# Kernel tuning notes

Measured on AMD Instinct MI355X. Metric: run time of the kernel, lower is better.

Reference implementation:

```python
import jax, jax.numpy as jnp
import numpy as np

B, S, D_IN = 2, 2048, 1024
D_OUT, HEADS = 1024, 16
HD = D_OUT // HEADS  # head_dim = 64


def rope_sincos(seq_len, head_dim):
    half = head_dim // 2
    inv_freq = 1.0 / (10000.0 ** (jnp.arange(half, dtype=jnp.float32) / half))
    angles = jnp.arange(seq_len, dtype=jnp.float32)[:, None] * inv_freq[None, :]  # (s, hd/2)
    return jnp.sin(angles), jnp.cos(angles)


def apply_rope(x, sin, cos):
    # x: (b, h, s, hd); interleaved-pair rotation as in the torch module
    b, h, s, hd = x.shape
    xp = x.reshape(b, h, s, hd // 2, 2)
    x0, x1 = xp[..., 0], xp[..., 1]
    sin = sin[:s][None, None, :, :]
    cos = cos[:s][None, None, :, :]
    r0 = x0 * cos - x1 * sin
    r1 = x0 * sin + x1 * cos
    return jnp.stack([r0, r1], axis=-1).reshape(b, h, s, hd)


def setup_inputs() -> dict:
    key = jax.random.key(0)
    kx, kq, kk, kv, ko = jax.random.split(key, 5)
    scale = 0.02
    return {
        "x": jax.random.normal(kx, (B, S, D_IN), dtype=jnp.float32),
        "Wq": jax.random.normal(kq, (D_IN, D_OUT), dtype=jnp.float32) * scale,
        "Wk": jax.random.normal(kk, (D_IN, D_OUT), dtype=jnp.float32) * scale,
        "Wv": jax.random.normal(kv, (D_IN, D_OUT), dtype=jnp.float32) * scale,
        "Wo": jax.random.normal(ko, (D_OUT, D_OUT), dtype=jnp.float32) * scale,
    }


def reference(x, Wq, Wk, Wv, Wo):
    b, s, _ = x.shape
    q = (x @ Wq).reshape(b, s, HEADS, HD).transpose(0, 2, 1, 3)  # (b,h,s,hd)
    k = (x @ Wk).reshape(b, s, HEADS, HD).transpose(0, 2, 1, 3)
    v = (x @ Wv).reshape(b, s, HEADS, HD).transpose(0, 2, 1, 3)
    sin, cos = rope_sincos(s, HD)
    q = apply_rope(q, sin, cos)
    k = apply_rope(k, sin, cos)
    scores = jnp.einsum('bhqd,bhkd->bhqk', q, k)
    causal = jnp.triu(jnp.ones((s, s), dtype=bool), 1)
    scores = jnp.where(causal[None, None], -jnp.inf, scores)
    weights = jax.nn.softmax(scores / jnp.sqrt(jnp.float32(HD)), axis=-1)
    ctx = jnp.einsum('bhqk,bhkd->bhqd', weights, v)
    ctx = ctx.transpose(0, 2, 1, 3).reshape(b, s, D_OUT)
    return ctx @ Wo
```

## Files before the change

### kernel.cpp

```cpp
#include <hip/hip_runtime.h>
#include <cstdint>
#include <cstddef>

#define BB 2
#define SS 2048
#define DD 1024
#define HH 16
#define HDD 64

typedef unsigned short u16;
typedef unsigned int u32;
typedef __attribute__((ext_vector_type(8))) short bf16x8;
typedef __attribute__((ext_vector_type(4))) float f32x4;

__device__ __forceinline__ u16 f2bf(float f) {
    union { float f; u32 u; } c; c.f = f;
    u32 r = c.u + 0x7fffu + ((c.u >> 16) & 1u);
    return (u16)(r >> 16);
}
__device__ __forceinline__ void gll16(const void* g, void* l) {
    __builtin_amdgcn_global_load_lds(
        (const __attribute__((address_space(1))) void*)g,
        (__attribute__((address_space(3))) void*)l, 16, 0, 0);
}

__global__ __launch_bounds__(256) void cvt_x(const float* __restrict__ X, u16* __restrict__ Xb)
{
    const int idx0 = blockIdx.x * 256 + threadIdx.x;
    #pragma unroll
    for (int i = 0; i < 4; i++) {
        const int c = idx0 + i * 262144;
        const float4 v = *(const float4*)&X[(size_t)c * 4];
        ushort4 o;
        o.x = f2bf(v.x); o.y = f2bf(v.y); o.z = f2bf(v.z); o.w = f2bf(v.w);
        *(ushort4*)&Xb[(size_t)c * 4] = o;
    }
}

__global__ __launch_bounds__(256) void trans_w4(
    const float* Wq, const float* Wk, const float* Wv, const float* Wo,
    u16* __restrict__ WTbase)
{
    __shared__ float L[32][33];
    const float* Ws[4] = {Wq, Wk, Wv, Wo};
    const float* W = Ws[blockIdx.z];
    u16* WT = WTbase + (size_t)blockIdx.z * (DD * DD);
    const int k0 = blockIdx.x * 32, n0 = blockIdx.y * 32;
    const int tx = threadIdx.x & 31, ty = threadIdx.x >> 5;
    #pragma unroll
    for (int i = 0; i < 4; i++)
        L[ty + 8 * i][tx] = W[(size_t)(k0 + ty + 8 * i) * DD + n0 + tx];
    __syncthreads();
    #pragma unroll
    for (int i = 0; i < 4; i++) {
        const int n = ty + 8 * i;
        WT[(size_t)(n0 + n) * DD + k0 + tx] = f2bf(L[tx][n]);
    }
}

__global__ __launch_bounds__(256) void gemm_qkv(
    const u16* __restrict__ Xb, const u16* __restrict__ WTall, u16* __restrict__ QKVb)
{
    __shared__ __align__(16) u16 sm[16384];
    const int tid = threadIdx.x;
    const int lane = tid & 63;
    const int w = tid >> 6;
    const int li = lane & 15, quad = lane >> 4;
    const int wr = w >> 1, wc = w & 1;
    const int which = blockIdx.x >> 3;
    const int n0 = (blockIdx.x & 7) * 128;
    const int m0 = blockIdx.y * 64;
    const u16* BT = WTall + (size_t)which * (DD * DD);
    u16* outp = QKVb + (size_t)which * ((size_t)BB * HH * SS * HDD);
    const float scale = (which == 0) ? 0.125f * 1.4426950408889634f : 1.0f;

    const int arow = tid >> 2;
    const int acol = (tid & 3) * 8;
    const int wbase = (tid >> 6) * 1024;

    auto stage = [&](int t, int buf) {
        char* base = (char*)(sm + buf * 6144);
        const int k0 = t * 32;
        gll16(Xb + (size_t)(m0 + arow) * DD + k0 + acol, base + wbase);
        #pragma unroll
        for (int rr = 0; rr < 2; rr++)
            gll16(BT + (size_t)(n0 + rr * 64 + arow) * DD + k0 + acol,
                  base + 4096 + rr * 4096 + wbase);
    };

    f32x4 acc[2][4] = {};
    stage(0, 0);
    __syncthreads();
    for (int t = 0; t < 32; t++) {
        const int buf = t & 1;
        if (t < 31) stage(t + 1, buf ^ 1);
        const u16* tA = sm + buf * 6144;
        const u16* tB = tA + 2048;
        bf16x8 a[2], b[4];
        #pragma unroll
        for (int f = 0; f < 2; f++)
            a[f] = *(const bf16x8*)(tA + (wr * 32 + f * 16 + li) * 32 + quad * 8);
        #pragma unroll
        for (int f = 0; f < 4; f++)
            b[f] = *(const bf16x8*)(tB + (wc * 64 + f * 16 + li) * 32 + quad * 8);
        #pragma unroll
        for (int fm = 0; fm < 2; fm++)
            #pragma unroll
            for (int fn = 0; fn < 4; fn++)
                acc[fm][fn] = __builtin_amdgcn_mfma_f32_16x16x32_bf16(
                    a[fm], b[fn], acc[fm][fn], 0, 0, 0);
        __syncthreads();
    }

    const int bidx = m0 >> 11;
    const int s0 = m0 & (SS - 1);
    if (which < 2) {
        float (*Ts)[128] = (float(*)[128])sm;
        #pragma unroll
        for (int fm = 0; fm < 2; fm++)
            #pragma unroll
            for (int fn = 0; fn < 4; fn++)
                #pragma unroll
                for (int r = 0; r < 4; r++)
                    Ts[wr * 32 + fm * 16 + quad * 4 + r][wc * 64 + fn * 16 + li] = acc[fm][fn][r];
        __syncthreads();
        #pragma unroll
        for (int i = 0; i < 4; i++) {
            const int c = tid + 256 * i;
            const int mr = c >> 4;
            const int nc = c & 15;
            const int s = s0 + mr;
            const int n = n0 + nc * 8;
            const int h = n >> 6, hd0 = n & 63;
            const float4 v0 = *(const float4*)&Ts[mr][nc * 8];
            const float4 v1 = *(const float4*)&Ts[mr][nc * 8 + 4];
            const float fs = (float)s;
            u32 w0, w1, w2, w3;
            {
                const float inv = exp2f((float)((hd0 >> 1) + 0) * -0.4152410118609203f);
                float sn, cs; sincosf(fs * inv, &sn, &cs);
                w0 = (u32)f2bf((v0.x * cs - v0.y * sn) * scale) |
                     ((u32)f2bf((v0.x * sn + v0.y * cs) * scale) << 16);
            }
            {
                const float inv = exp2f((float)((hd0 >> 1) + 1) * -0.4152410118609203f);
                float sn, cs; sincosf(fs * inv, &sn, &cs);
                w1 = (u32)f2bf((v0.z * cs - v0.w * sn) * scale) |
                     ((u32)f2bf((v0.z * sn + v0.w * cs) * scale) << 16);
            }
            {
                const float inv = exp2f((float)((hd0 >> 1) + 2) * -0.4152410118609203f);
                float sn, cs; sincosf(fs * inv, &sn, &cs);
                w2 = (u32)f2bf((v1.x * cs - v1.y * sn) * scale) |
                     ((u32)f2bf((v1.x * sn + v1.y * cs) * scale) << 16);
            }
            {
                const float inv = exp2f((float)((hd0 >> 1) + 3) * -0.4152410118609203f);
                float sn, cs; sincosf(fs * inv, &sn, &cs);
                w3 = (u32)f2bf((v1.z * cs - v1.w * sn) * scale) |
                     ((u32)f2bf((v1.z * sn + v1.w * cs) * scale) << 16);
            }
            uint4 ov; ov.x = w0; ov.y = w1; ov.z = w2; ov.w = w3;
            *(uint4*)&outp[((size_t)(bidx * HH + h) * SS + s) * HDD + hd0] = ov;
        }
    } else {
        float (*Ts)[64] = (float(*)[64])sm;
        #pragma unroll
        for (int fm = 0; fm < 2; fm++)
            #pragma unroll
            for (int fn = 0; fn < 4; fn++)
                *(float4*)&Ts[wc * 64 + fn * 16 + li][wr * 32 + fm * 16 + quad * 4] =
                    make_float4(acc[fm][fn][0], acc[fm][fn][1],
                                acc[fm][fn][2], acc[fm][fn][3]);
        __syncthreads();
        #pragma unroll
        for (int i = 0; i < 4; i++) {
            const int c = tid + 256 * i;
            const int nr = c >> 3;
            const int mc = c & 7;
            const int n = n0 + nr;
            const int h = n >> 6, hd = n & 63;
            const float4 v0 = *(const float4*)&Ts[nr][mc * 8];
            const float4 v1 = *(const float4*)&Ts[nr][mc * 8 + 4];
            uint4 ov;
            ov.x = (u32)f2bf(v0.x) | ((u32)f2bf(v0.y) << 16);
            ov.y = (u32)f2bf(v0.z) | ((u32)f2bf(v0.w) << 16);
            ov.z = (u32)f2bf(v1.x) | ((u32)f2bf(v1.y) << 16);
            ov.w = (u32)f2bf(v1.z) | ((u32)f2bf(v1.w) << 16);
            *(uint4*)&outp[((size_t)(bidx * HH + h) * HDD + hd) * SS + s0 + mc * 8] = ov;
        }
    }
}

__global__ __launch_bounds__(512) void attn_mfma(
    const u16* __restrict__ Qb, const u16* __restrict__ Kb,
    const u16* __restrict__ Vt, u16* __restrict__ ctxb)
{
    __shared__ u16 Ks[128][72];
    __shared__ u16 Vs[64][136];
    __shared__ u16 Ps[8][16][136];
    const int tid = threadIdx.x;
    const int lane = tid & 63;
    const int w = tid >> 6;
    const int li = lane & 15;
    const int quad = lane >> 4;
    const int bh = blockIdx.y;
    const int i = blockIdx.x;
    const int q0A = 128 * i;
    const int q0B = 128 * (15 - i);
    const int ntA = i + 1;
    const int ntB = 16 - i;

    bf16x8 aQA0, aQA1, aQB0, aQB1;
    {
        const u16* qa = Qb + ((size_t)bh * SS + q0A + 16 * w + li) * HDD + quad * 8;
        aQA0 = *(const bf16x8*)qa;
        aQA1 = *(const bf16x8*)(qa + 32);
        const u16* qb = Qb + ((size_t)bh * SS + q0B + 16 * w + li) * HDD + quad * 8;
        aQB0 = *(const bf16x8*)qb;
        aQB1 = *(const bf16x8*)(qb + 32);
    }

    f32x4 OA[4] = {}, OB[4] = {};
    float lA[4] = {}, lB[4] = {};

    const int kr = tid >> 2;
    const int kc = (tid & 3) * 16;
    const int vr = tid >> 3;
    const int vc = (tid & 7) * 16;

    auto process = [&](const bf16x8& aQ0, const bf16x8& aQ1,
                       f32x4 (&O)[4], float (&l_r)[4], const bool diag) {
        f32x4 S[8];
        #pragma unroll
        for (int t = 0; t < 8; t++) {
            const bf16x8 b0 = *(const bf16x8*)&Ks[16 * t + li][quad * 8];
            const bf16x8 b1 = *(const bf16x8*)&Ks[16 * t + li][32 + quad * 8];
            f32x4 a2 = {};
            a2 = __builtin_amdgcn_mfma_f32_16x16x32_bf16(aQ0, b0, a2, 0, 0, 0);
            a2 = __builtin_amdgcn_mfma_f32_16x16x32_bf16(aQ1, b1, a2, 0, 0, 0);
            S[t] = a2;
        }
        if (diag) {
            #pragma unroll
            for (int t = 0; t < 8; t++)
                #pragma unroll
                for (int r = 0; r < 4; r++)
                    if (16 * t + li > 16 * w + quad * 4 + r) S[t][r] = -1e30f;
        }
        float p[4][8];
        #pragma unroll
        for (int r = 0; r < 4; r++) {
            float ls = 0.f;
            #pragma unroll
            for (int t = 0; t < 8; t++) {
                p[r][t] = exp2f(S[t][r] - 8.0f);
                ls += p[r][t];
            }
            l_r[r] += ls;
        }
        #pragma unroll
        for (int r = 0; r < 4; r++)
            #pragma unroll
            for (int t = 0; t < 8; t++)
                Ps[w][quad * 4 + r][16 * t + li] = f2bf(p[r][t]);
        bf16x8 aP[4];
        #pragma unroll
        for (int c = 0; c < 4; c++)
            aP[c] = *(const bf16x8*)&Ps[w][li][32 * c + quad * 8];
        #pragma unroll
        for (int t2 = 0; t2 < 4; t2++) {
            #pragma unroll
            for (int c = 0; c < 4; c++) {
                const bf16x8 bv = *(const bf16x8*)&Vs[16 * t2 + li][32 * c + quad * 8];
                O[t2] = __builtin_amdgcn_mfma_f32_16x16x32_bf16(aP[c], bv, O[t2], 0, 0, 0);
            }
        }
    };

    for (int jt = 0; jt < ntB; jt++) {
        const int j0 = jt << 7;
        const uint4 k0v = *(const uint4*)(Kb + ((size_t)bh * SS + j0 + kr) * HDD + kc);
        const uint4 k1v = *(const uint4*)(Kb + ((size_t)bh * SS + j0 + kr) * HDD + kc + 8);
        const uint4 v0v = *(const uint4*)(Vt + ((size_t)bh * HDD + vr) * SS + j0 + vc);
        const uint4 v1v = *(const uint4*)(Vt + ((size_t)bh * HDD + vr) * SS + j0 + vc + 8);
        __syncthreads();
        *(uint4*)&Ks[kr][kc] = k0v;
        *(uint4*)&Ks[kr][kc + 8] = k1v;
        *(uint4*)&Vs[vr][vc] = v0v;
        *(uint4*)&Vs[vr][vc + 8] = v1v;
        __syncthreads();

        if (jt < ntA) process(aQA0, aQA1, OA, lA, jt == ntA - 1);
        process(aQB0, aQB1, OB, lB, jt == ntB - 1);
    }

    const int b = bh >> 4, h = bh & 15;
    #pragma unroll
    for (int r = 0; r < 4; r++) {
        float la = lA[r], lb = lB[r];
        #pragma unroll
        for (int off = 1; off < 16; off <<= 1) {
            la += __shfl_xor(la, off);
            lb += __shfl_xor(lb, off);
        }
        const float invA = 1.f / la;
        const float invB = 1.f / lb;
        const int rowA = q0A + 16 * w + quad * 4 + r;
        const int rowB = q0B + 16 * w + quad * 4 + r;
        #pragma unroll
        for (int t2 = 0; t2 < 4; t2++) {
            ctxb[((size_t)b * SS + rowA) * DD + h * HDD + 16 * t2 + li] = f2bf(OA[t2][r] * invA);
            ctxb[((size_t)b * SS + rowB) * DD + h * HDD + 16 * t2 + li] = f2bf(OB[t2][r] * invB);
        }
    }
}

__global__ __launch_bounds__(256) void gemm_out_mfma(
    const u16* __restrict__ Ab, const u16* __restrict__ WoT, float* __restrict__ out)
{
    __shared__ __align__(16) u16 sm[12288];
    const int tid = threadIdx.x;
    const int lane = tid & 63;
    const int w = tid >> 6;
    const int li = lane & 15, quad = lane >> 4;
    const int wr = w >> 1, wc = w & 1;
    const int n0 = blockIdx.x * 128;
    const int m0 = blockIdx.y * 64;

    const int arow = tid >> 2;
    const int acol = (tid & 3) * 8;
    const int wbase = (tid >> 6) * 1024;

    auto stage = [&](int t, int buf) {
        char* base = (char*)(sm + buf * 6144);
        const int k0 = t * 32;
        gll16(Ab + (size_t)(m0 + arow) * DD + k0 + acol, base + wbase);
        #pragma unroll
        for (int rr = 0; rr < 2; rr++)
            gll16(WoT + (size_t)(n0 + rr * 64 + arow) * DD + k0 + acol,
                  base + 4096 + rr * 4096 + wbase);
    };

    f32x4 acc[2][4] = {};
    stage(0, 0);
    __syncthreads();
    for (int t = 0; t < 32; t++) {
        const int buf = t & 1;
        if (t < 31) stage(t + 1, buf ^ 1);
        const u16* tA = sm + buf * 6144;
        const u16* tB = tA + 2048;
        bf16x8 a[2], b[4];
        #pragma unroll
        for (int f = 0; f < 2; f++)
            a[f] = *(const bf16x8*)(tA + (wr * 32 + f * 16 + li) * 32 + quad * 8);
        #pragma unroll
        for (int f = 0; f < 4; f++)
            b[f] = *(const bf16x8*)(tB + (wc * 64 + f * 16 + li) * 32 + quad * 8);
        #pragma unroll
        for (int fm = 0; fm < 2; fm++)
            #pragma unroll
            for (int fn = 0; fn < 4; fn++)
                acc[fm][fn] = __builtin_amdgcn_mfma_f32_16x16x32_bf16(
                    a[fm], b[fn], acc[fm][fn], 0, 0, 0);
        __syncthreads();
    }

    #pragma unroll
    for (int fm = 0; fm < 2; fm++)
        #pragma unroll
        for (int r = 0; r < 4; r++) {
            const size_t mg = (size_t)(m0 + wr * 32 + fm * 16 + quad * 4 + r) * DD;
            #pragma unroll
            for (int fn = 0; fn < 4; fn++)
                out[mg + n0 + wc * 64 + fn * 16 + li] = acc[fm][fn][r];
        }
}

extern "C" void kernel_launch(void* const* d_in, const int* in_sizes, int n_in,
                              void* d_out, int out_size, void* d_ws, size_t ws_size,
                              hipStream_t stream) {
    const float* x  = (const float*)d_in[0];
    const float* Wq = (const float*)d_in[1];
    const float* Wk = (const float*)d_in[2];
    const float* Wv = (const float*)d_in[3];
    const float* Wo = (const float*)d_in[4];
    float* out = (float*)d_out;

    u16* ws16 = (u16*)d_ws;
    const size_t E = 4194304;
    const size_t M = 1048576;
    u16* QKVb = ws16;
    u16* Qb   = QKVb;
    u16* Kb   = QKVb + E;
    u16* Vt   = QKVb + 2 * E;
    u16* Xb   = ws16 + 3 * E;
    u16* ctxb = Xb;
    u16* WTall = ws16 + 4 * E;
    u16* WoT  = WTall + 3 * M;

    hipLaunchKernelGGL(cvt_x, dim3(1024), dim3(256), 0, stream, x, Xb);
    hipLaunchKernelGGL(trans_w4, dim3(32, 32, 4), dim3(256), 0, stream,
                       Wq, Wk, Wv, Wo, WTall);
    hipLaunchKernelGGL(gemm_qkv, dim3(24, 64), dim3(256), 0, stream, Xb, WTall, QKVb);
    hipLaunchKernelGGL(attn_mfma, dim3(8, BB * HH), dim3(512), 0, stream,
                       Qb, Kb, Vt, ctxb);
    hipLaunchKernelGGL(gemm_out_mfma, dim3(8, 64), dim3(256), 0, stream, ctxb, WoT, out);
}
```

Before: 205.0 us.

## Use two waves per GEMM block with larger per-wave tiles and precomputed RoPE table

```diff
diff --git a/kernel.cpp b/kernel.cpp
--- a/kernel.cpp
+++ b/kernel.cpp
@@ -58,15 +58,14 @@
     }
 }
 
-__global__ __launch_bounds__(256) void gemm_qkv(
+__global__ __launch_bounds__(128) void gemm_qkv(
     const u16* __restrict__ Xb, const u16* __restrict__ WTall, u16* __restrict__ QKVb)
 {
     __shared__ __align__(16) u16 sm[16384];
     const int tid = threadIdx.x;
     const int lane = tid & 63;
-    const int w = tid >> 6;
+    const int w2 = tid >> 6;
     const int li = lane & 15, quad = lane >> 4;
-    const int wr = w >> 1, wc = w & 1;
     const int which = blockIdx.x >> 3;
     const int n0 = (blockIdx.x & 7) * 128;
     const int m0 = blockIdx.y * 64;
@@ -74,21 +73,24 @@
     u16* outp = QKVb + (size_t)which * ((size_t)BB * HH * SS * HDD);
     const float scale = (which == 0) ? 0.125f * 1.4426950408889634f : 1.0f;
 
-    const int arow = tid >> 2;
-    const int acol = (tid & 3) * 8;
-    const int wbase = (tid >> 6) * 1024;
+    const int srow = tid >> 2;
+    const int scol = (tid & 3) * 8;
+    const int wb = w2 * 1024;
 
     auto stage = [&](int t, int buf) {
-        char* base = (char*)(sm + buf * 6144);
+        char* base = (char*)sm + buf * 12288;
         const int k0 = t * 32;
-        gll16(Xb + (size_t)(m0 + arow) * DD + k0 + acol, base + wbase);
         #pragma unroll
         for (int rr = 0; rr < 2; rr++)
-            gll16(BT + (size_t)(n0 + rr * 64 + arow) * DD + k0 + acol,
-                  base + 4096 + rr * 4096 + wbase);
+            gll16(Xb + (size_t)(m0 + rr * 32 + srow) * DD + k0 + scol,
+                  base + rr * 2048 + wb);
+        #pragma unroll
+        for (int rr = 0; rr < 4; rr++)
+            gll16(BT + (size_t)(n0 + rr * 32 + srow) * DD + k0 + scol,
+                  base + 4096 + rr * 2048 + wb);
     };
 
-    f32x4 acc[2][4] = {};
+    f32x4 acc[4][4] = {};
     stage(0, 0);
     __syncthreads();
     for (int t = 0; t < 32; t++) {
@@ -96,15 +98,14 @@
         if (t < 31) stage(t + 1, buf ^ 1);
         const u16* tA = sm + buf * 6144;
         const u16* tB = tA + 2048;
-        bf16x8 a[2], b[4];
-        #pragma unroll
-        for (int f = 0; f < 2; f++)
-            a[f] = *(const bf16x8*)(tA + (wr * 32 + f * 16 + li) * 32 + quad * 8);
-        #pragma unroll
-        for (int f = 0; f < 4; f++)
-            b[f] = *(const bf16x8*)(tB + (wc * 64 + f * 16 + li) * 32 + quad * 8);
-        #pragma unroll
-        for (int fm = 0; fm < 2; fm++)
+        bf16x8 a[4], b[4];
+        #pragma unroll
+        for (int f = 0; f < 4; f++) {
+            a[f] = *(const bf16x8*)(tA + (f * 16 + li) * 32 + quad * 8);
+            b[f] = *(const bf16x8*)(tB + (w2 * 64 + f * 16 + li) * 32 + quad * 8);
+        }
+        #pragma unroll
+        for (int fm = 0; fm < 4; fm++)
             #pragma unroll
             for (int fn = 0; fn < 4; fn++)
                 acc[fm][fn] = __builtin_amdgcn_mfma_f32_16x16x32_bf16(
@@ -115,79 +116,93 @@
     const int bidx = m0 >> 11;
     const int s0 = m0 & (SS - 1);
     if (which < 2) {
+        float* tabc = (float*)(sm + 8192);
+        float* tabs = tabc + 2048;
+        {
+            const int j = tid & 31;
+            const int sb = tid >> 5;
+            const float inv = exp2f((float)j * -0.4152410118609203f);
+            #pragma unroll
+            for (int k = 0; k < 16; k++) {
+                const int sl = k * 4 + sb;
+                float sn, cs;
+                sincosf((float)(s0 + sl) * inv, &sn, &cs);
+                tabc[sl * 32 + j] = cs;
+                tabs[sl * 32 + j] = sn;
+            }
+        }
         float (*Ts)[128] = (float(*)[128])sm;
         #pragma unroll
-        for (int fm = 0; fm < 2; fm++)
-            #pragma unroll
-            for (int fn = 0; fn < 4; fn++)
+        for (int p = 0; p < 2; p++) {
+            if (p) __syncthreads();
+            #pragma unroll
+            for (int fm2 = 0; fm2 < 2; fm2++) {
+                const int fm = p * 2 + fm2;
                 #pragma unroll
-                for (int r = 0; r < 4; r++)
-                    Ts[wr * 32 + fm * 16 + quad * 4 + r][wc * 64 + fn * 16 + li] = acc[fm][fn][r];
-        __syncthreads();
-        #pragma unroll
-        for (int i = 0; i < 4; i++) {
-            const int c = tid + 256 * i;
-            const int mr = c >> 4;
-            const int nc = c & 15;
-            const int s = s0 + mr;
-            const int n = n0 + nc * 8;
-            const int h = n >> 6, hd0 = n & 63;
-            const float4 v0 = *(const float4*)&Ts[mr][nc * 8];
-            const float4 v1 = *(const float4*)&Ts[mr][nc * 8 + 4];
-            const float fs = (float)s;
-            u32 w0, w1, w2, w3;
-            {
-                const float inv = exp2f((float)((hd0 >> 1) + 0) * -0.4152410118609203f);
-                float sn, cs; sincosf(fs * inv, &sn, &cs);
-                w0 = (u32)f2bf((v0.x * cs - v0.y * sn) * scale) |
-                     ((u32)f2bf((v0.x * sn + v0.y * cs) * scale) << 16);
-            }
-            {
-                const float inv = exp2f((float)((hd0 >> 1) + 1) * -0.4152410118609203f);
-                float sn, cs; sincosf(fs * inv, &sn, &cs);
-                w1 = (u32)f2bf((v0.z * cs - v0.w * sn) * scale) |
-                     ((u32)f2bf((v0.z * sn + v0.w * cs) * scale) << 16);
-            }
-            {
-                const float inv = exp2f((float)((hd0 >> 1) + 2) * -0.4152410118609203f);
-                float sn, cs; sincosf(fs * inv, &sn, &cs);
-                w2 = (u32)f2bf((v1.x * cs - v1.y * sn) * scale) |
-                     ((u32)f2bf((v1.x * sn + v1.y * cs) * scale) << 16);
-            }
-            {
-                const float inv = exp2f((float)((hd0 >> 1) + 3) * -0.4152410118609203f);
-                float sn, cs; sincosf(fs * inv, &sn, &cs);
-                w3 = (u32)f2bf((v1.z * cs - v1.w * sn) * scale) |
-                     ((u32)f2bf((v1.z * sn + v1.w * cs) * scale) << 16);
-            }
-            uint4 ov; ov.x = w0; ov.y = w1; ov.z = w2; ov.w = w3;
-            *(uint4*)&outp[((size_t)(bidx * HH + h) * SS + s) * HDD + hd0] = ov;
+                for (int fn = 0; fn < 4; fn++)
+                    #pragma unroll
+                    for (int r = 0; r < 4; r++)
+                        Ts[fm2 * 16 + quad * 4 + r][w2 * 64 + fn * 16 + li] = acc[fm][fn][r];
+            }
+            __syncthreads();
+            #pragma unroll
+            for (int i = 0; i < 4; i++) {
+                const int c = tid + 128 * i;
+                const int mr = c >> 4;
+                const int nc = c & 15;
+                const int sl = p * 32 + mr;
+                const int s = s0 + sl;
+                const int n = n0 + nc * 8;
+                const int h = n >> 6, hd0 = n & 63;
+                const int j0 = hd0 >> 1;
+                const float4 v0 = *(const float4*)&Ts[mr][nc * 8];
+                const float4 v1 = *(const float4*)&Ts[mr][nc * 8 + 4];
+                const float4 cs4 = *(const float4*)&tabc[sl * 32 + j0];
+                const float4 sn4 = *(const float4*)&tabs[sl * 32 + j0];
+                u32 w0, w1, w2o, w3;
+                w0 = (u32)f2bf((v0.x * cs4.x - v0.y * sn4.x) * scale) |
+                     ((u32)f2bf((v0.x * sn4.x + v0.y * cs4.x) * scale) << 16);
+                w1 = (u32)f2bf((v0.z * cs4.y - v0.w * sn4.y) * scale) |
+                     ((u32)f2bf((v0.z * sn4.y + v0.w * cs4.y) * scale) << 16);
+                w2o = (u32)f2bf((v1.x * cs4.z - v1.y * sn4.z) * scale) |
+                      ((u32)f2bf((v1.x * sn4.z + v1.y * cs4.z) * scale) << 16);
+                w3 = (u32)f2bf((v1.z * cs4.w - v1.w * sn4.w) * scale) |
+                     ((u32)f2bf((v1.z * sn4.w + v1.w * cs4.w) * scale) << 16);
+                uint4 ov; ov.x = w0; ov.y = w1; ov.z = w2o; ov.w = w3;
+                *(uint4*)&outp[((size_t)(bidx * HH + h) * SS + s) * HDD + hd0] = ov;
+            }
         }
     } else {
         float (*Ts)[64] = (float(*)[64])sm;
         #pragma unroll
-        for (int fm = 0; fm < 2; fm++)
-            #pragma unroll
-            for (int fn = 0; fn < 4; fn++)
-                *(float4*)&Ts[wc * 64 + fn * 16 + li][wr * 32 + fm * 16 + quad * 4] =
-                    make_float4(acc[fm][fn][0], acc[fm][fn][1],
-                                acc[fm][fn][2], acc[fm][fn][3]);
-        __syncthreads();
-        #pragma unroll
-        for (int i = 0; i < 4; i++) {
-            const int c = tid + 256 * i;
-            const int nr = c >> 3;
-            const int mc = c & 7;
-            const int n = n0 + nr;
-            const int h = n >> 6, hd = n & 63;
-            const float4 v0 = *(const float4*)&Ts[nr][mc * 8];
-            const float4 v1 = *(const float4*)&Ts[nr][mc * 8 + 4];
-            uint4 ov;
-            ov.x = (u32)f2bf(v0.x) | ((u32)f2bf(v0.y) << 16);
-            ov.y = (u32)f2bf(v0.z) | ((u32)f2bf(v0.w) << 16);
-            ov.z = (u32)f2bf(v1.x) | ((u32)f2bf(v1.y) << 16);
-            ov.w = (u32)f2bf(v1.z) | ((u32)f2bf(v1.w) << 16);
-            *(uint4*)&outp[((size_t)(bidx * HH + h) * HDD + hd) * SS + s0 + mc * 8] = ov;
+        for (int p = 0; p < 2; p++) {
+            if (p) __syncthreads();
+            if (w2 == p) {
+                #pragma unroll
+                for (int fm = 0; fm < 4; fm++)
+                    #pragma unroll
+                    for (int fn = 0; fn < 4; fn++)
+                        *(float4*)&Ts[fn * 16 + li][fm * 16 + quad * 4] =
+                            make_float4(acc[fm][fn][0], acc[fm][fn][1],
+                                        acc[fm][fn][2], acc[fm][fn][3]);
+            }
+            __syncthreads();
+            #pragma unroll
+            for (int i = 0; i < 4; i++) {
+                const int c = tid + 128 * i;
+                const int nr = c >> 3;
+                const int mc = c & 7;
+                const int n = n0 + p * 64 + nr;
+                const int h = n >> 6, hd = n & 63;
+                const float4 v0 = *(const float4*)&Ts[nr][mc * 8];
+                const float4 v1 = *(const float4*)&Ts[nr][mc * 8 + 4];
+                uint4 ov;
+                ov.x = (u32)f2bf(v0.x) | ((u32)f2bf(v0.y) << 16);
+                ov.y = (u32)f2bf(v0.z) | ((u32)f2bf(v0.w) << 16);
+                ov.z = (u32)f2bf(v1.x) | ((u32)f2bf(v1.y) << 16);
+                ov.w = (u32)f2bf(v1.z) | ((u32)f2bf(v1.w) << 16);
+                *(uint4*)&outp[((size_t)(bidx * HH + h) * HDD + hd) * SS + s0 + mc * 8] = ov;
+            }
         }
     }
 }
@@ -316,33 +331,35 @@
     }
 }
 
-__global__ __launch_bounds__(256) void gemm_out_mfma(
+__global__ __launch_bounds__(128) void gemm_out_mfma(
     const u16* __restrict__ Ab, const u16* __restrict__ WoT, float* __restrict__ out)
 {
     __shared__ __align__(16) u16 sm[12288];
     const int tid = threadIdx.x;
     const int lane = tid & 63;
-    const int w = tid >> 6;
+    const int w2 = tid >> 6;
     const int li = lane & 15, quad = lane >> 4;
-    const int wr = w >> 1, wc = w & 1;
     const int n0 = blockIdx.x * 128;
     const int m0 = blockIdx.y * 64;
 
-    const int arow = tid >> 2;
-    const int acol = (tid & 3) * 8;
-    const int wbase = (tid >> 6) * 1024;
+    const int srow = tid >> 2;
+    const int scol = (tid & 3) * 8;
+    const int wb = w2 * 1024;
 
     auto stage = [&](int t, int buf) {
-        char* base = (char*)(sm + buf * 6144);
+        char* base = (char*)sm + buf * 12288;
         const int k0 = t * 32;
-        gll16(Ab + (size_t)(m0 + arow) * DD + k0 + acol, base + wbase);
         #pragma unroll
         for (int rr = 0; rr < 2; rr++)
-            gll16(WoT + (size_t)(n0 + rr * 64 + arow) * DD + k0 + acol,
-                  base + 4096 + rr * 4096 + wbase);
+            gll16(Ab + (size_t)(m0 + rr * 32 + srow) * DD + k0 + scol,
+                  base + rr * 2048 + wb);
+        #pragma unroll
+        for (int rr = 0; rr < 4; rr++)
+            gll16(WoT + (size_t)(n0 + rr * 32 + srow) * DD + k0 + scol,
+                  base + 4096 + rr * 2048 + wb);
     };
 
-    f32x4 acc[2][4] = {};
+    f32x4 acc[4][4] = {};
     stage(0, 0);
     __syncthreads();
     for (int t = 0; t < 32; t++) {
@@ -350,15 +367,14 @@
         if (t < 31) stage(t + 1, buf ^ 1);
         const u16* tA = sm + buf * 6144;
         const u16* tB = tA + 2048;
-        bf16x8 a[2], b[4];
-        #pragma unroll
-        for (int f = 0; f < 2; f++)
-            a[f] = *(const bf16x8*)(tA + (wr * 32 + f * 16 + li) * 32 + quad * 8);
-        #pragma unroll
-        for (int f = 0; f < 4; f++)
-            b[f] = *(const bf16x8*)(tB + (wc * 64 + f * 16 + li) * 32 + quad * 8);
-        #pragma unroll
-        for (int fm = 0; fm < 2; fm++)
+        bf16x8 a[4], b[4];
+        #pragma unroll
+        for (int f = 0; f < 4; f++) {
+            a[f] = *(const bf16x8*)(tA + (f * 16 + li) * 32 + quad * 8);
+            b[f] = *(const bf16x8*)(tB + (w2 * 64 + f * 16 + li) * 32 + quad * 8);
+        }
+        #pragma unroll
+        for (int fm = 0; fm < 4; fm++)
             #pragma unroll
             for (int fn = 0; fn < 4; fn++)
                 acc[fm][fn] = __builtin_amdgcn_mfma_f32_16x16x32_bf16(
@@ -367,13 +383,13 @@
     }
 
     #pragma unroll
-    for (int fm = 0; fm < 2; fm++)
+    for (int fm = 0; fm < 4; fm++)
         #pragma unroll
         for (int r = 0; r < 4; r++) {
-            const size_t mg = (size_t)(m0 + wr * 32 + fm * 16 + quad * 4 + r) * DD;
+            const size_t mg = (size_t)(m0 + fm * 16 + quad * 4 + r) * DD;
             #pragma unroll
             for (int fn = 0; fn < 4; fn++)
-                out[mg + n0 + wc * 64 + fn * 16 + li] = acc[fm][fn][r];
+                out[mg + n0 + w2 * 64 + fn * 16 + li] = acc[fm][fn][r];
         }
 }
 
@@ -402,8 +418,8 @@
     hipLaunchKernelGGL(cvt_x, dim3(1024), dim3(256), 0, stream, x, Xb);
     hipLaunchKernelGGL(trans_w4, dim3(32, 32, 4), dim3(256), 0, stream,
                        Wq, Wk, Wv, Wo, WTall);
-    hipLaunchKernelGGL(gemm_qkv, dim3(24, 64), dim3(256), 0, stream, Xb, WTall, QKVb);
+    hipLaunchKernelGGL(gemm_qkv, dim3(24, 64), dim3(128), 0, stream, Xb, WTall, QKVb);
     hipLaunchKernelGGL(attn_mfma, dim3(8, BB * HH), dim3(512), 0, stream,
                        Qb, Kb, Vt, ctxb);
-    hipLaunchKernelGGL(gemm_out_mfma, dim3(8, 64), dim3(256), 0, stream, ctxb, WoT, out);
-}
+    hipLaunchKernelGGL(gemm_out_mfma, dim3(8, 64), dim3(128), 0, stream, ctxb, WoT, out);
+}
```

Measured after the change: 218.6 us. 1.07x slower.
